# Kernel optimization log

Hardware: AMD Instinct MI355X
Metric: run time of the kernel (lower is better)

Reference implementation:

```python
import jax, jax.numpy as jnp
import numpy as np

D_MODEL = 1024
N_HEADS = 16
D_K = D_MODEL // N_HEADS
B, L = 2, 2048


def setup_inputs() -> dict:
    key = jax.random.key(0)
    ks = jax.random.split(key, 11)
    s = 1.0 / np.sqrt(D_MODEL)
    return {
        "q": jax.random.normal(ks[0], (B, L, D_MODEL), jnp.float32),
        "k": jax.random.normal(ks[1], (B, L, D_MODEL), jnp.float32),
        "v": jax.random.normal(ks[2], (B, L, D_MODEL), jnp.float32),
        "w_q": jax.random.normal(ks[3], (D_MODEL, D_MODEL), jnp.float32) * s,
        "b_q": jnp.zeros((D_MODEL,), jnp.float32),
        "w_k": jax.random.normal(ks[4], (D_MODEL, D_MODEL), jnp.float32) * s,
        "b_k": jnp.zeros((D_MODEL,), jnp.float32),
        "w_v": jax.random.normal(ks[5], (D_MODEL, D_MODEL), jnp.float32) * s,
        "b_v": jnp.zeros((D_MODEL,), jnp.float32),
        "w_o": jax.random.normal(ks[6], (D_MODEL, D_MODEL), jnp.float32) * s,
        "b_o": jnp.zeros((D_MODEL,), jnp.float32),
    }


def reference(q, k, v, w_q, b_q, w_k, b_k, w_v, b_v, w_o, b_o):
    b, l, _ = q.shape
    # QKV projections (flax Linear: x @ W + b)
    query = q @ w_q + b_q
    key_ = k @ w_k + b_k
    value = v @ w_v + b_v
    # (B, L, D) -> (B, H, L, d_k)
    query = query.reshape(b, l, N_HEADS, D_K).transpose(0, 2, 1, 3)
    key_ = key_.reshape(b, l, N_HEADS, D_K).transpose(0, 2, 1, 3)
    value = value.reshape(b, l, N_HEADS, D_K).transpose(0, 2, 1, 3)
    # scaled dot-product attention; full (B, H, L, L) score matrix per original
    scores = jnp.einsum("bhqd,bhkd->bhqk", query, key_) / jnp.sqrt(
        jnp.asarray(D_K, query.dtype)
    )
    attn = jax.nn.softmax(scores, axis=-1)
    x = jnp.einsum("bhqk,bhkd->bhqd", attn, value)
    # (B, H, L, d_k) -> (B, L, D)
    x = x.transpose(0, 2, 1, 3).reshape(b, l, D_MODEL)
    return x @ w_o + b_o
```

## Files before the change

### kernel.cpp

```cpp
#include <hip/hip_runtime.h>
#include <hip/hip_bf16.h>


#define D_MODELC 1024
#define N_HEADSC 16
#define D_KC 64
#define BBC 2
#define LLC 2048
#define MMC (BBC * LLC)

typedef __attribute__((ext_vector_type(8))) short v8s;
typedef __attribute__((ext_vector_type(4))) float v4f;

__device__ __forceinline__ float bf2f(unsigned short u) {
    union { unsigned int i; float f; } x;
    x.i = ((unsigned int)u) << 16;
    return x.f;
}
__device__ __forceinline__ unsigned short f2bf(float f) {
    union { float f; unsigned int i; } x;
    x.f = f;
    unsigned int r = x.i + 0x7fffu + ((x.i >> 16) & 1u);
    return (unsigned short)(r >> 16);
}
__device__ __forceinline__ unsigned int pk2bf(float a, float b) {
    __hip_bfloat162 h = __float22bfloat162_rn(make_float2(a, b));
    return *(unsigned int*)&h;
}

#define AS1 __attribute__((address_space(1)))
#define AS3 __attribute__((address_space(3)))

__global__ __launch_bounds__(256) void wtrans(const float* __restrict__ w0,
                                              const float* __restrict__ w1,
                                              const float* __restrict__ w2,
                                              const float* __restrict__ w3,
                                              unsigned short* __restrict__ out) {
    __shared__ unsigned short T[64][65];
    const int z = blockIdx.z;
    const float* W = z == 0 ? w0 : (z == 1 ? w1 : (z == 2 ? w2 : w3));
    unsigned short* O = out + (size_t)z * D_MODELC * D_MODELC;
    const int k0 = blockIdx.y * 64, n0 = blockIdx.x * 64;
    const int c = threadIdx.x & 63, r4 = threadIdx.x >> 6;
#pragma unroll
    for (int i = 0; i < 16; i++) {
        int r = i * 4 + r4;
        T[r][c] = f2bf(W[(size_t)(k0 + r) * D_MODELC + n0 + c]);
    }
    __syncthreads();
#pragma unroll
    for (int i = 0; i < 16; i++) {
        int r = i * 4 + r4;
        O[(size_t)(n0 + r) * D_MODELC + k0 + c] = T[c][r];
    }
}

__global__ __launch_bounds__(256) void vtrans(const unsigned short* __restrict__ Vp,
                                              unsigned short* __restrict__ Vt) {
    __shared__ __align__(16) unsigned short T[64][68];
    const int bh = blockIdx.y;
    const int b = bh >> 4, h = bh & 15;
    const int j0 = blockIdx.x * 64;
    const int t = threadIdx.x;
#pragma unroll
    for (int i = 0; i < 2; i++) {
        int c = i * 256 + t;
        int row = c >> 3, ch = c & 7;
        *(v8s*)&T[row][ch * 8] =
            *(const v8s*)&Vp[((size_t)(b * LLC + j0 + row)) * D_MODELC + h * 64 + ch * 8];
    }
    __syncthreads();
#pragma unroll
    for (int i = 0; i < 2; i++) {
        int c = i * 256 + t;
        int drow = c >> 3, jch = c & 7;
        v8s pk;
#pragma unroll
        for (int u = 0; u < 8; u++) pk[u] = (short)T[jch * 8 + u][drow];
        *(v8s*)&Vt[((size_t)bh * 64 + drow) * LLC + j0 + jch * 8] = pk;
    }
}

template <int MT, int SEGS, bool A_F32, bool OUT_F32>
__global__ __launch_bounds__(256) void gemm_tile(
    const void* __restrict__ A0, const void* __restrict__ A1, const void* __restrict__ A2,
    const unsigned short* __restrict__ Wt,
    const float* __restrict__ bias0, const float* __restrict__ bias1,
    const float* __restrict__ bias2,
    void* __restrict__ C0, void* __restrict__ C1, void* __restrict__ C2,
    float scale0, float scale1, float scale2) {
    const int K = D_MODELC, N = D_MODELC;
    constexpr int MI = MT / 32;
    constexpr int MB = MMC / MT;
    constexpr int PER = SEGS * MB / 8;
    __shared__ __align__(16) unsigned short As[MT * 32];
    __shared__ __align__(16) unsigned short Bs[128 * 32];

    const int t = threadIdx.x;
    const int w = t >> 6, lane = t & 63;
    const int quad = lane >> 4, m15 = lane & 15;
    const int wr = w >> 1, wc = w & 1;

    const int flat = blockIdx.x;
    const int xcd = flat & 7;
    const int slot = flat >> 3;
    const int group = xcd * PER + (slot >> 3);
    const int nb = slot & 7;
    const int seg = group / MB;
    const int mb = group % MB;
    const int n0 = nb * 128;
    const int m0 = mb * MT;

    const void* Ap = seg == 0 ? A0 : (seg == 1 ? A1 : A2);
    const unsigned short* Wp = Wt + (size_t)seg * D_MODELC * D_MODELC;
    const float* bias = seg == 0 ? bias0 : (seg == 1 ? bias1 : bias2);
    void* Cp = seg == 0 ? C0 : (seg == 1 ? C1 : C2);
    const float scl = seg == 0 ? scale0 : (seg == 1 ? scale1 : scale2);

    v4f acc[MI][4];
#pragma unroll
    for (int mi = 0; mi < MI; mi++)
#pragma unroll
        for (int ni = 0; ni < 4; ni++) acc[mi][ni] = (v4f){0.f, 0.f, 0.f, 0.f};

    for (int k0 = 0; k0 < K; k0 += 32) {
#pragma unroll
        for (int i = 0; i < 2; i++) {
            int c = i * 256 + t;
            int row = c >> 2, cc = (c & 3) * 8;
            const unsigned short* g = Wp + (size_t)(n0 + row) * K + k0 + cc;
            __builtin_amdgcn_global_load_lds(
                (const AS1 unsigned int*)g,
                (AS3 unsigned int*)(Bs + i * 2048 + w * 512), 16, 0, 0);
        }
        if (A_F32) {
#pragma unroll
            for (int i = 0; i < MT / 64; i++) {
                int c = i * 256 + t;
                int row = c >> 2, cc = (c & 3) * 8;
                const float* src = (const float*)Ap + (size_t)(m0 + row) * K + k0 + cc;
                float4 f0 = ((const float4*)src)[0];
                float4 f1 = ((const float4*)src)[1];
                uint4 pk;
                pk.x = pk2bf(f0.x, f0.y);
                pk.y = pk2bf(f0.z, f0.w);
                pk.z = pk2bf(f1.x, f1.y);
                pk.w = pk2bf(f1.z, f1.w);
                *(uint4*)&As[c * 8] = pk;
            }
        } else {
#pragma unroll
            for (int i = 0; i < MT / 64; i++) {
                int c = i * 256 + t;
                int row = c >> 2, cc = (c & 3) * 8;
                const unsigned short* g =
                    (const unsigned short*)Ap + (size_t)(m0 + row) * K + k0 + cc;
                __builtin_amdgcn_global_load_lds(
                    (const AS1 unsigned int*)g,
                    (AS3 unsigned int*)(As + i * 2048 + w * 512), 16, 0, 0);
            }
        }
        __syncthreads();

        v8s a[MI], b[4];
#pragma unroll
        for (int mi = 0; mi < MI; mi++)
            a[mi] = *(const v8s*)&As[(wr * (MT / 2) + mi * 16 + m15) * 32 + quad * 8];
#pragma unroll
        for (int ni = 0; ni < 4; ni++)
            b[ni] = *(const v8s*)&Bs[(wc * 64 + ni * 16 + m15) * 32 + quad * 8];
#pragma unroll
        for (int mi = 0; mi < MI; mi++)
#pragma unroll
            for (int ni = 0; ni < 4; ni++)
                acc[mi][ni] =
                    __builtin_amdgcn_mfma_f32_16x16x32_bf16(a[mi], b[ni], acc[mi][ni], 0, 0, 0);
        __syncthreads();
    }

#pragma unroll
    for (int ni = 0; ni < 4; ni++) {
        int col = n0 + wc * 64 + ni * 16 + m15;
        float bv = bias[col];
#pragma unroll
        for (int mi = 0; mi < MI; mi++) {
#pragma unroll
            for (int r = 0; r < 4; r++) {
                int row = m0 + wr * (MT / 2) + mi * 16 + quad * 4 + r;
                float v = (acc[mi][ni][r] + bv) * scl;
                if (OUT_F32)
                    ((float*)Cp)[(size_t)row * N + col] = v;
                else
                    ((unsigned short*)Cp)[(size_t)row * N + col] = f2bf(v);
            }
        }
    }
}

__global__ __launch_bounds__(256) void attn_mfma(const unsigned short* __restrict__ Qp,
                                                 const unsigned short* __restrict__ Kp,
                                                 const unsigned short* __restrict__ Vt,
                                                 unsigned short* __restrict__ X) {
    __shared__ __align__(16) unsigned short lds[8192 + 8192 + 128 * 72];
    unsigned short* Kb = lds;
    unsigned short* Vb = lds + 8192;
    unsigned short* PQ = lds + 16384;

    const int t = threadIdx.x;
    const int w = t >> 6, lane = t & 63;
    const int quad = lane >> 4, m15 = lane & 15;
    const int bh = blockIdx.y;
    const int b = bh >> 4, h = bh & 15;
    const int q0 = blockIdx.x * 128;
    const size_t hd = (size_t)h * 64;
    const int sw = m15 & 7;

#pragma unroll
    for (int i = 0; i < 4; i++) {
        int chunk = i * 256 + t;
        int row = chunk >> 3, slot = chunk & 7;
        int j = slot ^ (row & 7);
        const unsigned short* g =
            Qp + ((size_t)(b * LLC + q0 + row)) * D_MODELC + hd + j * 8;
        __builtin_amdgcn_global_load_lds((const AS1 unsigned int*)g,
                                         (AS3 unsigned int*)(PQ + (i * 256 + w * 64) * 8),
                                         16, 0, 0);
    }
    {
#pragma unroll
        for (int i = 0; i < 2; i++) {
            int chunk = i * 256 + t;
            int row = chunk >> 3, slot = chunk & 7;
            int j = slot ^ (row & 7);
            int gr = 4 * (row & 15) + (row >> 4);
            const unsigned short* g =
                Kp + ((size_t)(b * LLC + 0 + gr)) * D_MODELC + hd + j * 8;
            __builtin_amdgcn_global_load_lds((const AS1 unsigned int*)g,
                                             (AS3 unsigned int*)(Kb + (i * 256 + w * 64) * 8),
                                             16, 0, 0);
        }
#pragma unroll
        for (int i = 0; i < 2; i++) {
            int chunk = i * 256 + t;
            int row = chunk >> 3, slot = chunk & 7;
            int j = slot ^ (row & 7);
            const unsigned short* g = Vt + ((size_t)(bh * 64 + row)) * LLC + 0 + j * 8;
            __builtin_amdgcn_global_load_lds((const AS1 unsigned int*)g,
                                             (AS3 unsigned int*)(Vb + (i * 256 + w * 64) * 8),
                                             16, 0, 0);
        }
    }
    __syncthreads();

    v8s qa[2][2];
#pragma unroll
    for (int mi = 0; mi < 2; mi++)
#pragma unroll
        for (int kk = 0; kk < 2; kk++)
            qa[mi][kk] = *(const v8s*)&PQ[(w * 32 + mi * 16 + m15) * 64 +
                                          (((kk * 4 + quad) ^ sw) * 8)];
    __syncthreads();

    v8s ones;
#pragma unroll
    for (int u = 0; u < 8; u++) ones[u] = (short)0x3F80;

    v4f O[2][4];
#pragma unroll
    for (int mi = 0; mi < 2; mi++)
#pragma unroll
        for (int db = 0; db < 4; db++) O[mi][db] = (v4f){0.f, 0.f, 0.f, 0.f};
    v4f lacc[2] = {(v4f){0.f, 0.f, 0.f, 0.f}, (v4f){0.f, 0.f, 0.f, 0.f}};

    for (int it = 0; it < 32; it++) {
        const int cur = it & 1;
        unsigned short* Kc = Kb + cur * 4096;
        unsigned short* Vc = Vb + cur * 4096;
        if (it < 31) {
            unsigned short* Kn = Kb + (cur ^ 1) * 4096;
            unsigned short* Vn = Vb + (cur ^ 1) * 4096;
            const int k0n = (it + 1) * 64;
#pragma unroll
            for (int i = 0; i < 2; i++) {
                int chunk = i * 256 + t;
                int row = chunk >> 3, slot = chunk & 7;
                int j = slot ^ (row & 7);
                int gr = 4 * (row & 15) + (row >> 4);
                const unsigned short* g =
                    Kp + ((size_t)(b * LLC + k0n + gr)) * D_MODELC + hd + j * 8;
                __builtin_amdgcn_global_load_lds(
                    (const AS1 unsigned int*)g,
                    (AS3 unsigned int*)(Kn + (i * 256 + w * 64) * 8), 16, 0, 0);
            }
#pragma unroll
            for (int i = 0; i < 2; i++) {
                int chunk = i * 256 + t;
                int row = chunk >> 3, slot = chunk & 7;
                int j = slot ^ (row & 7);
                const unsigned short* g =
                    Vt + ((size_t)(bh * 64 + row)) * LLC + k0n + j * 8;
                __builtin_amdgcn_global_load_lds(
                    (const AS1 unsigned int*)g,
                    (AS3 unsigned int*)(Vn + (i * 256 + w * 64) * 8), 16, 0, 0);
            }
        }

        v4f S[2][4];
#pragma unroll
        for (int mi = 0; mi < 2; mi++)
#pragma unroll
            for (int ns = 0; ns < 4; ns++) S[mi][ns] = (v4f){0.f, 0.f, 0.f, 0.f};
#pragma unroll
        for (int kk = 0; kk < 2; kk++) {
#pragma unroll
            for (int ns = 0; ns < 4; ns++) {
                v8s kf = *(const v8s*)&Kc[(ns * 16 + m15) * 64 +
                                          (((kk * 4 + quad) ^ sw) * 8)];
#pragma unroll
                for (int mi = 0; mi < 2; mi++)
                    S[mi][ns] =
                        __builtin_amdgcn_mfma_f32_16x16x32_bf16(qa[mi][kk], kf, S[mi][ns], 0, 0, 0);
            }
        }

#pragma unroll
        for (int mi = 0; mi < 2; mi++) {
#pragma unroll
            for (int r = 0; r < 4; r++) {
                int prow = w * 32 + mi * 16 + quad * 4 + r;
                float e0 = __builtin_amdgcn_exp2f(S[mi][0][r]);
                float e1 = __builtin_amdgcn_exp2f(S[mi][1][r]);
                float e2 = __builtin_amdgcn_exp2f(S[mi][2][r]);
                float e3 = __builtin_amdgcn_exp2f(S[mi][3][r]);
                uint2 pk;
                pk.x = pk2bf(e0, e1);
                pk.y = pk2bf(e2, e3);
                *(uint2*)&PQ[prow * 72 + 4 * m15] = pk;
            }
        }

#pragma unroll
        for (int kk = 0; kk < 2; kk++) {
            v8s a0 = *(const v8s*)&PQ[(w * 32 + 0 * 16 + m15) * 72 + kk * 32 + quad * 8];
            v8s a1 = *(const v8s*)&PQ[(w * 32 + 1 * 16 + m15) * 72 + kk * 32 + quad * 8];
            lacc[0] = __builtin_amdgcn_mfma_f32_16x16x32_bf16(a0, ones, lacc[0], 0, 0, 0);
            lacc[1] = __builtin_amdgcn_mfma_f32_16x16x32_bf16(a1, ones, lacc[1], 0, 0, 0);
#pragma unroll
            for (int db = 0; db < 4; db++) {
                v8s vf = *(const v8s*)&Vc[(db * 16 + m15) * 64 +
                                          (((kk * 4 + quad) ^ sw) * 8)];
                O[0][db] = __builtin_amdgcn_mfma_f32_16x16x32_bf16(a0, vf, O[0][db], 0, 0, 0);
                O[1][db] = __builtin_amdgcn_mfma_f32_16x16x32_bf16(a1, vf, O[1][db], 0, 0, 0);
            }
        }
        __syncthreads();
    }

#pragma unroll
    for (int mi = 0; mi < 2; mi++) {
#pragma unroll
        for (int r = 0; r < 4; r++) {
            float inv = 1.f / lacc[mi][r];
            int row = q0 + w * 32 + mi * 16 + quad * 4 + r;
#pragma unroll
            for (int db = 0; db < 4; db++) {
                X[((size_t)(b * LLC + row)) * D_MODELC + hd + db * 16 + m15] =
                    f2bf(O[mi][db][r] * inv);
            }
        }
    }
}

extern "C" void kernel_launch(void* const* d_in, const int* in_sizes, int n_in,
                              void* d_out, int out_size, void* d_ws, size_t ws_size,
                              hipStream_t stream) {
    const float* q = (const float*)d_in[0];
    const float* k = (const float*)d_in[1];
    const float* v = (const float*)d_in[2];
    const float* w_q = (const float*)d_in[3];
    const float* b_q = (const float*)d_in[4];
    const float* w_k = (const float*)d_in[5];
    const float* b_k = (const float*)d_in[6];
    const float* w_v = (const float*)d_in[7];
    const float* b_v = (const float*)d_in[8];
    const float* w_o = (const float*)d_in[9];
    const float* b_o = (const float*)d_in[10];

    const size_t elems = (size_t)MMC * D_MODELC;
    unsigned short* Qp = (unsigned short*)d_ws;
    unsigned short* Kp = Qp + elems;
    unsigned short* Vp = Kp + elems;
    unsigned short* Wt = Vp + elems;
    unsigned short* X = Qp;
    unsigned short* Vt = (unsigned short*)d_out;

    const float QSCALE = 0.125f * 1.44269504088896340736f;

    wtrans<<<dim3(16, 16, 4), 256, 0, stream>>>(w_q, w_k, w_v, w_o, Wt);

    gemm_tile<128, 3, true, false><<<768, 256, 0, stream>>>(
        q, k, v, Wt, b_q, b_k, b_v, Qp, Kp, Vp, QSCALE, 1.f, 1.f);

    vtrans<<<dim3(LLC / 64, BBC * N_HEADSC), 256, 0, stream>>>(Vp, Vt);

    attn_mfma<<<dim3(LLC / 128, BBC * N_HEADSC), 256, 0, stream>>>(Qp, Kp, Vt, X);

    gemm_tile<64, 1, false, true><<<512, 256, 0, stream>>>(
        X, X, X, Wt + (size_t)3 * D_MODELC * D_MODELC, b_o, b_o, b_o,
        d_out, d_out, d_out, 1.f, 1.f, 1.f);
}
```

Before: 244.1 us.

## Double-buffer LDS tiles in projection GEMM to overlap loads with MFMA

The QKV and output projection GEMMs now use two LDS buffers for A and B. The next k-slice is prefetched, through async global_load_lds or register loads of fp32 A, while MFMAs run on the current slice. This removes one barrier per iteration and hides global load latency. In exchange it doubles shared memory use and adds registers for the prefetched fp32 values, which may lower occupancy.

```diff
diff --git a/kernel.cpp b/kernel.cpp
--- a/kernel.cpp
+++ b/kernel.cpp
@@ -93,8 +93,8 @@
     constexpr int MI = MT / 32;
     constexpr int MB = MMC / MT;
     constexpr int PER = SEGS * MB / 8;
-    __shared__ __align__(16) unsigned short As[MT * 32];
-    __shared__ __align__(16) unsigned short Bs[128 * 32];
+    __shared__ __align__(16) unsigned short As[2][MT * 32];
+    __shared__ __align__(16) unsigned short Bs[2][128 * 32];
 
     const int t = threadIdx.x;
     const int w = t >> 6, lane = t & 63;
@@ -117,13 +117,31 @@
     void* Cp = seg == 0 ? C0 : (seg == 1 ? C1 : C2);
     const float scl = seg == 0 ? scale0 : (seg == 1 ? scale1 : scale2);
 
-    v4f acc[MI][4];
-#pragma unroll
-    for (int mi = 0; mi < MI; mi++)
-#pragma unroll
-        for (int ni = 0; ni < 4; ni++) acc[mi][ni] = (v4f){0.f, 0.f, 0.f, 0.f};
-
-    for (int k0 = 0; k0 < K; k0 += 32) {
+    float4 fa[MT / 64][2];
+
+    auto loadA = [&](int k0) {
+#pragma unroll
+        for (int i = 0; i < MT / 64; i++) {
+            int c = i * 256 + t;
+            int row = c >> 2, cc = (c & 3) * 8;
+            const float* src = (const float*)Ap + (size_t)(m0 + row) * K + k0 + cc;
+            fa[i][0] = ((const float4*)src)[0];
+            fa[i][1] = ((const float4*)src)[1];
+        }
+    };
+    auto convA = [&](int buf) {
+#pragma unroll
+        for (int i = 0; i < MT / 64; i++) {
+            int c = i * 256 + t;
+            uint4 pk;
+            pk.x = pk2bf(fa[i][0].x, fa[i][0].y);
+            pk.y = pk2bf(fa[i][0].z, fa[i][0].w);
+            pk.z = pk2bf(fa[i][1].x, fa[i][1].y);
+            pk.w = pk2bf(fa[i][1].z, fa[i][1].w);
+            *(uint4*)&As[buf][c * 8] = pk;
+        }
+    };
+    auto stageB = [&](int k0, int buf) {
 #pragma unroll
         for (int i = 0; i < 2; i++) {
             int c = i * 256 + t;
@@ -131,50 +149,57 @@
             const unsigned short* g = Wp + (size_t)(n0 + row) * K + k0 + cc;
             __builtin_amdgcn_global_load_lds(
                 (const AS1 unsigned int*)g,
-                (AS3 unsigned int*)(Bs + i * 2048 + w * 512), 16, 0, 0);
-        }
-        if (A_F32) {
-#pragma unroll
-            for (int i = 0; i < MT / 64; i++) {
-                int c = i * 256 + t;
-                int row = c >> 2, cc = (c & 3) * 8;
-                const float* src = (const float*)Ap + (size_t)(m0 + row) * K + k0 + cc;
-                float4 f0 = ((const float4*)src)[0];
-                float4 f1 = ((const float4*)src)[1];
-                uint4 pk;
-                pk.x = pk2bf(f0.x, f0.y);
-                pk.y = pk2bf(f0.z, f0.w);
-                pk.z = pk2bf(f1.x, f1.y);
-                pk.w = pk2bf(f1.z, f1.w);
-                *(uint4*)&As[c * 8] = pk;
-            }
-        } else {
-#pragma unroll
-            for (int i = 0; i < MT / 64; i++) {
-                int c = i * 256 + t;
-                int row = c >> 2, cc = (c & 3) * 8;
-                const unsigned short* g =
-                    (const unsigned short*)Ap + (size_t)(m0 + row) * K + k0 + cc;
-                __builtin_amdgcn_global_load_lds(
-                    (const AS1 unsigned int*)g,
-                    (AS3 unsigned int*)(As + i * 2048 + w * 512), 16, 0, 0);
-            }
-        }
-        __syncthreads();
-
-        v8s a[MI], b[4];
+                (AS3 unsigned int*)(&Bs[buf][0] + i * 2048 + w * 512), 16, 0, 0);
+        }
+    };
+    auto stageA_async = [&](int k0, int buf) {
+#pragma unroll
+        for (int i = 0; i < MT / 64; i++) {
+            int c = i * 256 + t;
+            int row = c >> 2, cc = (c & 3) * 8;
+            const unsigned short* g =
+                (const unsigned short*)Ap + (size_t)(m0 + row) * K + k0 + cc;
+            __builtin_amdgcn_global_load_lds(
+                (const AS1 unsigned int*)g,
+                (AS3 unsigned int*)(&As[buf][0] + i * 2048 + w * 512), 16, 0, 0);
+        }
+    };
+
+    v4f acc[MI][4];
+#pragma unroll
+    for (int mi = 0; mi < MI; mi++)
+#pragma unroll
+        for (int ni = 0; ni < 4; ni++) acc[mi][ni] = (v4f){0.f, 0.f, 0.f, 0.f};
+
+    if (A_F32) loadA(0);
+    stageB(0, 0);
+    if (A_F32) convA(0); else stageA_async(0, 0);
+    __syncthreads();
+
+    for (int it = 0; it < K / 32; it++) {
+        const int cur = it & 1;
+        const bool more = it < K / 32 - 1;
+        if (more) {
+            if (A_F32) loadA((it + 1) * 32);
+            stageB((it + 1) * 32, cur ^ 1);
+            if (!A_F32) stageA_async((it + 1) * 32, cur ^ 1);
+        }
+
+        v8s a[MI], bfr[4];
 #pragma unroll
         for (int mi = 0; mi < MI; mi++)
-            a[mi] = *(const v8s*)&As[(wr * (MT / 2) + mi * 16 + m15) * 32 + quad * 8];
+            a[mi] = *(const v8s*)&As[cur][(wr * (MT / 2) + mi * 16 + m15) * 32 + quad * 8];
 #pragma unroll
         for (int ni = 0; ni < 4; ni++)
-            b[ni] = *(const v8s*)&Bs[(wc * 64 + ni * 16 + m15) * 32 + quad * 8];
+            bfr[ni] = *(const v8s*)&Bs[cur][(wc * 64 + ni * 16 + m15) * 32 + quad * 8];
 #pragma unroll
         for (int mi = 0; mi < MI; mi++)
 #pragma unroll
             for (int ni = 0; ni < 4; ni++)
                 acc[mi][ni] =
-                    __builtin_amdgcn_mfma_f32_16x16x32_bf16(a[mi], b[ni], acc[mi][ni], 0, 0, 0);
+                    __builtin_amdgcn_mfma_f32_16x16x32_bf16(a[mi], bfr[ni], acc[mi][ni], 0, 0, 0);
+
+        if (more && A_F32) convA(cur ^ 1);
         __syncthreads();
     }
 
```

Measured after the change: 253.3 us. 1.04x slower.
